# Kernel tuning notes

Hardware: AMD Instinct MI355X
Metric: run time of the kernel (lower is better)

Reference implementation:

```python
import jax, jax.numpy as jnp
import numpy as np

B, H, V, MSG_MAX_LEN = 16384, 512, 32, 20


def setup_inputs() -> dict:
    key = jax.random.key(0)
    ks = jax.random.split(key, 8)
    s = 0.05  # weight scale so softmax stays well-conditioned
    return {
        "encoder_hidden": jax.random.normal(ks[0], (B, H), jnp.float32),
        "encoder_cell": jax.random.normal(ks[1], (B, H), jnp.float32),
        "W_ih": jax.random.normal(ks[2], (4 * H, V), jnp.float32) * s,
        "b_ih": jax.random.normal(ks[3], (4 * H,), jnp.float32) * s,
        "W_hh": jax.random.normal(ks[4], (4 * H, H), jnp.float32) * s,
        "b_hh": jax.random.normal(ks[5], (4 * H,), jnp.float32) * s,
        "W_out": jax.random.normal(ks[6], (V, H), jnp.float32) * s,
        "b_out": jax.random.normal(ks[7], (V,), jnp.float32) * s,
        "init_input": jnp.zeros((1, V), jnp.float32),
        "eos_idx": 31,
    }


def reference(encoder_hidden, encoder_cell, W_ih, b_ih, W_hh, b_hh, W_out, b_out, init_input, eos_idx):
    batch = encoder_hidden.shape[0]
    vocab = W_out.shape[0]
    # Original code never updates decoder_input (typo 'deocder_input'), so the
    # LSTM input is init_input every step -> input projection is loop-invariant.
    x = jnp.broadcast_to(init_input, (batch, init_input.shape[1]))
    x_proj = x @ W_ih.T + b_ih  # [B, 4H]

    def step(carry, _):
        h, c, mask, lp = carry  # h,c: [B,H]; mask: [1,B]; lp: scalar
        mask_out = mask  # mask is appended BEFORE the update in the original
        gates = x_proj + h @ W_hh.T + b_hh
        i, f, g, o = jnp.split(gates, 4, axis=1)  # torch LSTMCell gate order i,f,g,o
        i = jax.nn.sigmoid(i); f = jax.nn.sigmoid(f)
        g = jnp.tanh(g); o = jax.nn.sigmoid(o)
        c = f * c + i * g
        h = o * jnp.tanh(c)
        probs = jax.nn.softmax(h @ W_out.T + b_out, axis=1)  # [B,V]
        predict = jax.nn.one_hot(jnp.argmax(probs, axis=1), vocab, dtype=probs.dtype)  # eval-mode branch
        lp = lp + jnp.log((probs * predict).sum(axis=1)) @ mask[0]
        new_mask = mask * (1.0 - predict[:, eos_idx])  # zero out finished sequences
        return (h, c, new_mask, lp), (predict, mask_out)

    init = (encoder_hidden, encoder_cell,
            jnp.ones((1, batch), encoder_hidden.dtype),
            jnp.zeros((), encoder_hidden.dtype))
    (_, _, _, log_probs), (message, mask) = jax.lax.scan(step, init, None, length=MSG_MAX_LEN)
    return message, mask, log_probs  # [L,B,V], [L,1,B], scalar
```

## Files before the change

kernel.cpp:

```cpp
#include <hip/hip_runtime.h>
#include <math.h>

#define BATCH 16384
#define HDIM  512
#define VOCAB 32
#define STEPS 20
#define G4    2048

typedef _Float16 f16;
typedef _Float16 f16x8 __attribute__((ext_vector_type(8)));
typedef float    f32x16 __attribute__((ext_vector_type(16)));

#define SH   256.0f
#define SW   1024.0f
#define SINV (1.0f / (SH * SW))


__device__ __forceinline__ void gload16(const void* g, void* l) {
#if defined(__has_builtin) && __has_builtin(__builtin_amdgcn_global_load_lds)
    __builtin_amdgcn_global_load_lds(
        (const __attribute__((address_space(1))) void*)g,
        (__attribute__((address_space(3))) void*)l, 16, 0, 0);
#else
    *(float4*)l = *(const float4*)g;
#endif
}

__device__ __forceinline__ float fsig(float x)  { return 1.0f / (1.0f + __expf(-x)); }
__device__ __forceinline__ float ftanh(float x) { return 1.0f - 2.0f / (__expf(2.0f * x) + 1.0f); }

__global__ void init_xb_kernel(const float* __restrict__ W_ih,
                               const float* __restrict__ b_ih,
                               const float* __restrict__ b_hh,
                               const float* __restrict__ x0,
                               float* __restrict__ xb) {
    int n = blockIdx.x * blockDim.x + threadIdx.x;
    if (n >= G4) return;
    float s = b_ih[n] + b_hh[n];
    const float* wr = W_ih + (size_t)n * VOCAB;
    #pragma unroll
    for (int v = 0; v < VOCAB; v++) s += wr[v] * x0[v];
    xb[n] = s;
}

__global__ void init_mask_kernel(float* __restrict__ mask) {
    int b = blockIdx.x * blockDim.x + threadIdx.x;
    if (b < BATCH) mask[b] = 1.0f;
}

__global__ void wimg_kernel(const float* __restrict__ W_hh,
                            f16* __restrict__ Wh, f16* __restrict__ Wl) {
    size_t g  = (size_t)blockIdx.x * 256 + threadIdx.x;
    int ln = g & 63;  size_t r = g >> 6;
    int gg = r & 3;   size_t r2 = r >> 2;
    int ks = r2 & 1;  size_t r3 = r2 >> 1;
    int kc = r3 & 15; int jb = (int)(r3 >> 4);
    int n = gg * 512 + jb * 32 + (ln & 31);
    int k = kc * 32 + ks * 16 + (ln >> 5) * 8;
    const float* s = W_hh + (size_t)n * HDIM + k;
    f16x8 vh, vl;
    #pragma unroll
    for (int i = 0; i < 8; i++) {
        float x = s[i] * SW;
        f16 h = (f16)x;
        vh[i] = h;
        vl[i] = (f16)(x - (float)h);
    }
    *(f16x8*)(Wh + g * 8) = vh;
    *(f16x8*)(Wl + g * 8) = vl;
}

__global__ void woutimg_kernel(const float* __restrict__ W_out,
                               f16* __restrict__ Oh, f16* __restrict__ Ol) {
    int g  = blockIdx.x * 256 + threadIdx.x;
    int ln = g & 63;
    int r  = g >> 6;
    int kc = r >> 1, ks = r & 1;
    int v  = ln & 31;
    int k  = kc * 32 + ks * 16 + (ln >> 5) * 8;
    const float* s = W_out + (size_t)v * HDIM + k;
    f16x8 vh, vl;
    #pragma unroll
    for (int i = 0; i < 8; i++) {
        float x = s[i] * SW;
        f16 h = (f16)x;
        vh[i] = h;
        vl[i] = (f16)(x - (float)h);
    }
    *(f16x8*)(Oh + (size_t)g * 8) = vh;
    *(f16x8*)(Ol + (size_t)g * 8) = vl;
}

__global__ void hT_init_kernel(const float* __restrict__ src,
                               f16* __restrict__ dh, f16* __restrict__ dl) {
    size_t g = (size_t)blockIdx.x * 256 + threadIdx.x;
    int ln = g & 63;  size_t r = g >> 6;
    int mb = (int)(r & 511); int kk = (int)(r >> 9);
    int m = mb * 32 + (ln & 31);
    int k = kk * 16 + (ln >> 5) * 8;
    const float* s = src + (size_t)m * HDIM + k;
    f16x8 vh, vl;
    #pragma unroll
    for (int i = 0; i < 8; i++) {
        float x = s[i] * SH;
        f16 h = (f16)x;
        vh[i] = h;
        vl[i] = (f16)(x - (float)h);
    }
    *(f16x8*)(dh + g * 8) = vh;
    *(f16x8*)(dl + g * 8) = vl;
}

__global__ __launch_bounds__(256, 2)
void gemm_cell_mfma(const f16* __restrict__ hT_h, const f16* __restrict__ hT_l,
                    f16* __restrict__ hTo_h, f16* __restrict__ hTo_l,
                    float* __restrict__ c,
                    const f16* __restrict__ Wimg_h, const f16* __restrict__ Wimg_l,
                    const float* __restrict__ xb) {
    __shared__ __align__(16) char smem_raw[34048];
    f16* Blds = (f16*)smem_raw;

    const int tid  = threadIdx.x;
    const int lane = tid & 63;
    const int wave = tid >> 6;
    const int wm   = wave;
    const int spw  = wave >> 1;
    const int ksw  = wave & 1;
    const int jb   = blockIdx.y;
    const int mb0  = blockIdx.x * 8;
    const int m0   = blockIdx.x * 256;
    const int j0   = jb * 32;
    const int half = lane >> 5;
    const int l31  = lane & 31;

    f32x16 acc[2][4];
    #pragma unroll
    for (int t = 0; t < 2; t++)
        #pragma unroll
        for (int g = 0; g < 4; g++)
            #pragma unroll
            for (int r = 0; r < 16; r++) acc[t][g][r] = 0.0f;

    const f16* bsrc0 = (spw ? Wimg_l : Wimg_h)
                     + ((size_t)jb * 128 + ksw * 4) * 512 + lane * 8;
    f16* bdst0 = Blds + (size_t)(spw * 8 + ksw * 4) * 512 + lane * 8;

    auto stage_b = [&](int kc, int buf) {
        const f16* s = bsrc0 + (size_t)kc * 4096;
        f16* d = bdst0 + buf * 16 * 512;
        #pragma unroll
        for (int g = 0; g < 4; g++)
            gload16(s + g * 512, d + g * 512);
    };

    const size_t abase0 = ((size_t)mb0 + wm * 2) * 512 + lane * 8;
    auto load_ah = [&](int kc, f16x8 (&dst)[2][2]) {
        #pragma unroll
        for (int ks = 0; ks < 2; ks++)
            #pragma unroll
            for (int t = 0; t < 2; t++)
                dst[ks][t] = *(const f16x8*)(hT_h + abase0
                               + (size_t)(kc * 2 + ks) * (512 * 512) + t * 512);
    };
    auto load_al = [&](int kc, f16x8 (&dst)[2][2]) {
        #pragma unroll
        for (int ks = 0; ks < 2; ks++)
            #pragma unroll
            for (int t = 0; t < 2; t++)
                dst[ks][t] = *(const f16x8*)(hT_l + abase0
                               + (size_t)(kc * 2 + ks) * (512 * 512) + t * 512);
    };

    auto compute = [&](f16x8 (&ah)[2][2], f16x8 (&al)[2][2], int buf) {
        #pragma unroll
        for (int ks = 0; ks < 2; ks++) {
            f16x8 bh[4], bl[4];
            #pragma unroll
            for (int g = 0; g < 4; g++) {
                bh[g] = *(const f16x8*)(Blds + (size_t)(buf * 16 + ks * 4 + g) * 512 + lane * 8);
                bl[g] = *(const f16x8*)(Blds + (size_t)(buf * 16 + 8 + ks * 4 + g) * 512 + lane * 8);
            }
            #pragma unroll
            for (int g = 0; g < 4; g++)
                #pragma unroll
                for (int t = 0; t < 2; t++) {
                    acc[t][g] = __builtin_amdgcn_mfma_f32_32x32x16_f16(ah[ks][t], bh[g], acc[t][g], 0, 0, 0);
                    acc[t][g] = __builtin_amdgcn_mfma_f32_32x32x16_f16(ah[ks][t], bl[g], acc[t][g], 0, 0, 0);
                }
            #pragma unroll
            for (int g = 0; g < 4; g++)
                #pragma unroll
                for (int t = 0; t < 2; t++)
                    acc[t][g] = __builtin_amdgcn_mfma_f32_32x32x16_f16(al[ks][t], bh[g], acc[t][g], 0, 0, 0);
        }
    };

    f16x8 ah0[2][2], ah1[2][2], al[2][2];
    stage_b(0, 0);
    load_ah(0, ah0);
    for (int kc2 = 0; kc2 < 8; kc2++) {
        const int kc = kc2 * 2;
        __syncthreads();
        stage_b(kc + 1, 1);
        load_ah(kc + 1, ah1);
        load_al(kc, al);
        compute(ah0, al, 0);
        __syncthreads();
        stage_b(kc + 2, 0);
        load_ah(kc + 2, ah0);
        load_al(kc + 1, al);
        compute(ah1, al, 1);
    }

    __syncthreads();
    unsigned int* hstage = (unsigned int*)smem_raw;

    const float xbi = xb[0 * HDIM + j0 + l31];
    const float xbf = xb[1 * HDIM + j0 + l31];
    const float xbg = xb[2 * HDIM + j0 + l31];
    const float xbo = xb[3 * HDIM + j0 + l31];
    #pragma unroll
    for (int t = 0; t < 2; t++) {
        #pragma unroll
        for (int reg = 0; reg < 16; reg++) {
            int row = (reg & 3) + 8 * (reg >> 2) + 4 * half;
            int ml  = wm * 64 + t * 32 + row;
            float gi = acc[t][0][reg] * SINV + xbi;
            float gf = acc[t][1][reg] * SINV + xbf;
            float gg = acc[t][2][reg] * SINV + xbg;
            float go = acc[t][3][reg] * SINV + xbo;
            float si = fsig(gi);
            float sf = fsig(gf);
            float tg = ftanh(gg);
            float so = fsig(go);
            size_t idx = (size_t)(m0 + ml) * HDIM + j0 + l31;
            float cn = sf * c[idx] + si * tg;
            c[idx] = cn;
            float hs = so * ftanh(cn) * SH;
            f16 hh = (f16)hs;
            f16 hl = (f16)(hs - (float)hh);
            union { f16 h[2]; unsigned int u; } pk;
            pk.h[0] = hh; pk.h[1] = hl;
            hstage[ml * 33 + l31] = pk.u;
        }
    }
    __syncthreads();

    #pragma unroll
    for (int s = 0; s < 4; s++) {
        int q   = tid + s * 256;
        int ksp = q >> 9;
        int mbl = (q >> 6) & 7;
        int ln  = q & 63;
        int mrow = mbl * 32 + (ln & 31);
        int jj8  = ksp * 16 + (ln >> 5) * 8;
        f16x8 vh, vl;
        #pragma unroll
        for (int i = 0; i < 8; i++) {
            union { unsigned int u; f16 h[2]; } pk;
            pk.u = hstage[mrow * 33 + jj8 + i];
            vh[i] = pk.h[0];
            vl[i] = pk.h[1];
        }
        size_t gq = ((size_t)(jb * 2 + ksp) * 512 + mb0 + mbl) * 64 + ln;
        *(f16x8*)(hTo_h + gq * 8) = vh;
        *(f16x8*)(hTo_l + gq * 8) = vl;
    }
}

__global__ __launch_bounds__(64)
void out_mfma(const f16* __restrict__ hTh, const f16* __restrict__ hTl,
              const f16* __restrict__ Oh, const f16* __restrict__ Ol,
              const float* __restrict__ b_out,
              float* __restrict__ mask,
              float* __restrict__ msg_t,
              float* __restrict__ maskout_t,
              float* __restrict__ lp_part,
              const int* __restrict__ eos_ptr) {
    const int lane = threadIdx.x;
    const int mb   = blockIdx.x;
    const int half = lane >> 5;
    const int l31  = lane & 31;

    f32x16 acc;
    #pragma unroll
    for (int r = 0; r < 16; r++) acc[r] = 0.0f;

    f16x8 ah[3][2], al[3][2], bh[3][2], bl[3][2];
    auto load_frags = [&](int kc, int buf) {
        #pragma unroll
        for (int ks = 0; ks < 2; ks++) {
            size_t ga = ((size_t)(kc * 2 + ks) * 512 + mb) * 64 + lane;
            size_t gb = ((size_t)(kc * 2 + ks)) * 64 + lane;
            ah[buf][ks] = *(const f16x8*)(hTh + ga * 8);
            al[buf][ks] = *(const f16x8*)(hTl + ga * 8);
            bh[buf][ks] = *(const f16x8*)(Oh + gb * 8);
            bl[buf][ks] = *(const f16x8*)(Ol + gb * 8);
        }
    };

    load_frags(0, 0);
    load_frags(1, 1);
    for (int kc = 0; kc < 16; kc++) {
        load_frags(kc + 2, (kc + 2) % 3);
        int b = kc % 3;
        #pragma unroll
        for (int ks = 0; ks < 2; ks++) {
            acc = __builtin_amdgcn_mfma_f32_32x32x16_f16(ah[b][ks], bh[b][ks], acc, 0, 0, 0);
            acc = __builtin_amdgcn_mfma_f32_32x32x16_f16(ah[b][ks], bl[b][ks], acc, 0, 0, 0);
            acc = __builtin_amdgcn_mfma_f32_32x32x16_f16(al[b][ks], bh[b][ks], acc, 0, 0, 0);
        }
    }

    const float bo  = b_out[l31];
    const int   eos = *eos_ptr;
    const int   m0  = mb * 32;
    float lpacc = 0.0f;

    #pragma unroll
    for (int reg = 0; reg < 16; reg++) {
        int row = (reg & 3) + 8 * (reg >> 2) + 4 * half;
        int m   = m0 + row;
        float logit = acc[reg] * SINV + bo;

        float mval = logit;
        int   midx = l31;
        #pragma unroll
        for (int off = 16; off > 0; off >>= 1) {
            float ov = __shfl_xor(mval, off, 32);
            int   oi = __shfl_xor(midx, off, 32);
            if (ov > mval || (ov == mval && oi < midx)) { mval = ov; midx = oi; }
        }
        float s = __expf(logit - mval);
        #pragma unroll
        for (int off = 16; off > 0; off >>= 1) s += __shfl_xor(s, off, 32);

        msg_t[(size_t)m * VOCAB + l31] = (l31 == midx) ? 1.0f : 0.0f;
        if (l31 == 0) {
            float mo = mask[m];
            maskout_t[m] = mo;
            lpacc += mo * (-__logf(s));
            if (midx == eos) mask[m] = 0.0f;
        }
    }
    lpacc += __shfl_xor(lpacc, 32);
    if (lane == 0) lp_part[mb] = lpacc;
}

__global__ void reduce_lp_kernel(const float* __restrict__ parts, int n,
                                 float* __restrict__ out) {
    __shared__ float sm[256];
    float s = 0.0f;
    for (int i = threadIdx.x; i < n; i += 256) s += parts[i];
    sm[threadIdx.x] = s;
    __syncthreads();
    for (int off = 128; off > 0; off >>= 1) {
        if (threadIdx.x < off) sm[threadIdx.x] += sm[threadIdx.x + off];
        __syncthreads();
    }
    if (threadIdx.x == 0) *out = sm[0];
}

extern "C" void kernel_launch(void* const* d_in, const int* in_sizes, int n_in,
                              void* d_out, int out_size, void* d_ws, size_t ws_size,
                              hipStream_t stream) {
    const float* enc_h  = (const float*)d_in[0];
    const float* enc_c  = (const float*)d_in[1];
    const float* W_ih   = (const float*)d_in[2];
    const float* b_ih   = (const float*)d_in[3];
    const float* W_hh   = (const float*)d_in[4];
    const float* b_hh   = (const float*)d_in[5];
    const float* W_out  = (const float*)d_in[6];
    const float* b_out  = (const float*)d_in[7];
    const float* x0     = (const float*)d_in[8];
    const int*   eosP   = (const int*)d_in[9];

    float* out     = (float*)d_out;
    float* msg     = out;
    float* maskout = out + (size_t)STEPS * BATCH * VOCAB;
    float* lp_out  = maskout + (size_t)STEPS * BATCH;

    const size_t NH = (size_t)BATCH * HDIM;
    char* w = (char*)d_ws;
    f16* hTh_a = (f16*)w;            w += NH * sizeof(f16);
    f16* hTl_a = (f16*)w;            w += NH * sizeof(f16);
    f16* hTh_b = (f16*)w;            w += NH * sizeof(f16);
    f16* hTl_b = (f16*)w;            w += NH * sizeof(f16);
    float* cbuf = (float*)w;         w += NH * sizeof(float);
    f16* Wimg_h = (f16*)w;           w += (size_t)G4 * HDIM * sizeof(f16);
    f16* Wimg_l = (f16*)w;           w += (size_t)G4 * HDIM * sizeof(f16);
    f16* Wout_h = (f16*)w;           w += (size_t)VOCAB * HDIM * sizeof(f16);
    f16* Wout_l = (f16*)w;           w += (size_t)VOCAB * HDIM * sizeof(f16);
    float* xb = (float*)w;           w += G4 * sizeof(float);
    float* maskbuf = (float*)w;      w += BATCH * sizeof(float);
    float* lp_parts = (float*)w;

    hipMemcpyAsync(cbuf, enc_c, NH * sizeof(float), hipMemcpyDeviceToDevice, stream);
    init_mask_kernel<<<(BATCH + 255) / 256, 256, 0, stream>>>(maskbuf);
    init_xb_kernel<<<(G4 + 255) / 256, 256, 0, stream>>>(W_ih, b_ih, b_hh, x0, xb);
    wimg_kernel<<<(G4 * HDIM / 8) / 256, 256, 0, stream>>>(W_hh, Wimg_h, Wimg_l);
    woutimg_kernel<<<8, 256, 0, stream>>>(W_out, Wout_h, Wout_l);
    hT_init_kernel<<<(int)((NH / 8) / 256), 256, 0, stream>>>(enc_h, hTh_a, hTl_a);

    for (int t = 0; t < STEPS; t++) {
        const f16* hi_in = (t & 1) ? hTh_b : hTh_a;
        const f16* lo_in = (t & 1) ? hTl_b : hTl_a;
        f16* hi_out      = (t & 1) ? hTh_a : hTh_b;
        f16* lo_out      = (t & 1) ? hTl_a : hTl_b;
        gemm_cell_mfma<<<dim3(BATCH / 256, HDIM / 32), 256, 0, stream>>>(
            hi_in, lo_in, hi_out, lo_out, cbuf, Wimg_h, Wimg_l, xb);
        out_mfma<<<BATCH / 32, 64, 0, stream>>>(
            hi_out, lo_out, Wout_h, Wout_l, b_out, maskbuf,
            msg + (size_t)t * BATCH * VOCAB,
            maskout + (size_t)t * BATCH,
            lp_parts + (size_t)t * (BATCH / 32),
            eosP);
    }
    reduce_lp_kernel<<<1, 256, 0, stream>>>(lp_parts, STEPS * (BATCH / 32), lp_out);
}
```

Before: 2.641 ms.

## Fuse output projection of previous step into next step's LSTM gemm launch

Merges the per-step gemm_cell and out_mfma kernels into one launch. Extra blocks compute the vocab projection, argmax and log-prob for step t-1 while the main blocks compute the LSTM cell for step t, since both only read the previous hidden state. This halves the launch count and lets the small, low-occupancy output work overlap the large GEMM. It also bounds the fragment prefetch in the output loop, which previously loaded past the last chunk, and reorders the MFMA issue order in the gemm. One trailing output launch handles the final step. The risk is that output blocks compete with gemm blocks for CUs.

Result: faster. 2.570 ms (-2.7%).

```diff
diff --git a/kernel.cpp b/kernel.cpp
--- a/kernel.cpp
+++ b/kernel.cpp
@@ -111,24 +111,116 @@
     *(f16x8*)(dl + g * 8) = vl;
 }
 
+__device__ __forceinline__ void out_body(int lane, int mb,
+        const f16* __restrict__ hTh, const f16* __restrict__ hTl,
+        const f16* __restrict__ Oh,  const f16* __restrict__ Ol,
+        const float* __restrict__ b_out,
+        float* __restrict__ mask, float* __restrict__ msg_t,
+        float* __restrict__ maskout_t, float* __restrict__ lp_part, int eos) {
+    const int half = lane >> 5;
+    const int l31  = lane & 31;
+
+    f32x16 acc;
+    #pragma unroll
+    for (int r = 0; r < 16; r++) acc[r] = 0.0f;
+
+    f16x8 ah[3][2], al[3][2], bh[3][2], bl[3][2];
+    auto load_frags = [&](int kc, int buf) {
+        #pragma unroll
+        for (int ks = 0; ks < 2; ks++) {
+            size_t ga = ((size_t)(kc * 2 + ks) * 512 + mb) * 64 + lane;
+            size_t gb = ((size_t)(kc * 2 + ks)) * 64 + lane;
+            ah[buf][ks] = *(const f16x8*)(hTh + ga * 8);
+            al[buf][ks] = *(const f16x8*)(hTl + ga * 8);
+            bh[buf][ks] = *(const f16x8*)(Oh + gb * 8);
+            bl[buf][ks] = *(const f16x8*)(Ol + gb * 8);
+        }
+    };
+
+    load_frags(0, 0);
+    load_frags(1, 1);
+    for (int kc = 0; kc < 16; kc++) {
+        if (kc < 14) load_frags(kc + 2, (kc + 2) % 3);
+        int b = kc % 3;
+        #pragma unroll
+        for (int ks = 0; ks < 2; ks++) {
+            acc = __builtin_amdgcn_mfma_f32_32x32x16_f16(ah[b][ks], bh[b][ks], acc, 0, 0, 0);
+            acc = __builtin_amdgcn_mfma_f32_32x32x16_f16(ah[b][ks], bl[b][ks], acc, 0, 0, 0);
+            acc = __builtin_amdgcn_mfma_f32_32x32x16_f16(al[b][ks], bh[b][ks], acc, 0, 0, 0);
+        }
+    }
+
+    const float bo = b_out[l31];
+    const int   m0 = mb * 32;
+    float lpacc = 0.0f;
+
+    #pragma unroll
+    for (int reg = 0; reg < 16; reg++) {
+        int row = (reg & 3) + 8 * (reg >> 2) + 4 * half;
+        int m   = m0 + row;
+        float logit = acc[reg] * SINV + bo;
+
+        float mval = logit;
+        int   midx = l31;
+        #pragma unroll
+        for (int off = 16; off > 0; off >>= 1) {
+            float ov = __shfl_xor(mval, off, 32);
+            int   oi = __shfl_xor(midx, off, 32);
+            if (ov > mval || (ov == mval && oi < midx)) { mval = ov; midx = oi; }
+        }
+        float s = __expf(logit - mval);
+        #pragma unroll
+        for (int off = 16; off > 0; off >>= 1) s += __shfl_xor(s, off, 32);
+
+        msg_t[(size_t)m * VOCAB + l31] = (l31 == midx) ? 1.0f : 0.0f;
+        if (l31 == 0) {
+            float mo = mask[m];
+            maskout_t[m] = mo;
+            lpacc += mo * (-__logf(s));
+            if (midx == eos) mask[m] = 0.0f;
+        }
+    }
+    lpacc += __shfl_xor(lpacc, 32);
+    if (lane == 0) lp_part[mb] = lpacc;
+}
+
 __global__ __launch_bounds__(256, 2)
-void gemm_cell_mfma(const f16* __restrict__ hT_h, const f16* __restrict__ hT_l,
-                    f16* __restrict__ hTo_h, f16* __restrict__ hTo_l,
-                    float* __restrict__ c,
-                    const f16* __restrict__ Wimg_h, const f16* __restrict__ Wimg_l,
-                    const float* __restrict__ xb) {
+void step_fused(const f16* __restrict__ hT_h, const f16* __restrict__ hT_l,
+                f16* __restrict__ hTo_h, f16* __restrict__ hTo_l,
+                float* __restrict__ c,
+                const f16* __restrict__ Wimg_h, const f16* __restrict__ Wimg_l,
+                const float* __restrict__ xb,
+                const f16* __restrict__ Oh, const f16* __restrict__ Ol,
+                const float* __restrict__ b_out,
+                float* __restrict__ mask,
+                float* __restrict__ msg_p,
+                float* __restrict__ maskout_p,
+                float* __restrict__ lp_p,
+                const int* __restrict__ eos_ptr,
+                int has_out) {
     __shared__ __align__(16) char smem_raw[34048];
     f16* Blds = (f16*)smem_raw;
 
     const int tid  = threadIdx.x;
     const int lane = tid & 63;
     const int wave = tid >> 6;
+    const int bid  = blockIdx.x;
+
+    if (bid >= 1024) {
+        if (!has_out) return;
+        int mb = (bid - 1024) * 4 + wave;
+        out_body(lane, mb, hT_h, hT_l, Oh, Ol, b_out,
+                 mask, msg_p, maskout_p, lp_p, *eos_ptr);
+        return;
+    }
+
     const int wm   = wave;
     const int spw  = wave >> 1;
     const int ksw  = wave & 1;
-    const int jb   = blockIdx.y;
-    const int mb0  = blockIdx.x * 8;
-    const int m0   = blockIdx.x * 256;
+    const int jb   = bid >> 6;
+    const int mt64 = bid & 63;
+    const int mb0  = mt64 * 8;
+    const int m0   = mt64 * 256;
     const int j0   = jb * 32;
     const int half = lane >> 5;
     const int l31  = lane & 31;
@@ -183,10 +275,13 @@
             #pragma unroll
             for (int g = 0; g < 4; g++)
                 #pragma unroll
-                for (int t = 0; t < 2; t++) {
+                for (int t = 0; t < 2; t++)
                     acc[t][g] = __builtin_amdgcn_mfma_f32_32x32x16_f16(ah[ks][t], bh[g], acc[t][g], 0, 0, 0);
+            #pragma unroll
+            for (int g = 0; g < 4; g++)
+                #pragma unroll
+                for (int t = 0; t < 2; t++)
                     acc[t][g] = __builtin_amdgcn_mfma_f32_32x32x16_f16(ah[ks][t], bl[g], acc[t][g], 0, 0, 0);
-                }
             #pragma unroll
             for (int g = 0; g < 4; g++)
                 #pragma unroll
@@ -277,74 +372,8 @@
               float* __restrict__ maskout_t,
               float* __restrict__ lp_part,
               const int* __restrict__ eos_ptr) {
-    const int lane = threadIdx.x;
-    const int mb   = blockIdx.x;
-    const int half = lane >> 5;
-    const int l31  = lane & 31;
-
-    f32x16 acc;
-    #pragma unroll
-    for (int r = 0; r < 16; r++) acc[r] = 0.0f;
-
-    f16x8 ah[3][2], al[3][2], bh[3][2], bl[3][2];
-    auto load_frags = [&](int kc, int buf) {
-        #pragma unroll
-        for (int ks = 0; ks < 2; ks++) {
-            size_t ga = ((size_t)(kc * 2 + ks) * 512 + mb) * 64 + lane;
-            size_t gb = ((size_t)(kc * 2 + ks)) * 64 + lane;
-            ah[buf][ks] = *(const f16x8*)(hTh + ga * 8);
-            al[buf][ks] = *(const f16x8*)(hTl + ga * 8);
-            bh[buf][ks] = *(const f16x8*)(Oh + gb * 8);
-            bl[buf][ks] = *(const f16x8*)(Ol + gb * 8);
-        }
-    };
-
-    load_frags(0, 0);
-    load_frags(1, 1);
-    for (int kc = 0; kc < 16; kc++) {
-        load_frags(kc + 2, (kc + 2) % 3);
-        int b = kc % 3;
-        #pragma unroll
-        for (int ks = 0; ks < 2; ks++) {
-            acc = __builtin_amdgcn_mfma_f32_32x32x16_f16(ah[b][ks], bh[b][ks], acc, 0, 0, 0);
-            acc = __builtin_amdgcn_mfma_f32_32x32x16_f16(ah[b][ks], bl[b][ks], acc, 0, 0, 0);
-            acc = __builtin_amdgcn_mfma_f32_32x32x16_f16(al[b][ks], bh[b][ks], acc, 0, 0, 0);
-        }
-    }
-
-    const float bo  = b_out[l31];
-    const int   eos = *eos_ptr;
-    const int   m0  = mb * 32;
-    float lpacc = 0.0f;
-
-    #pragma unroll
-    for (int reg = 0; reg < 16; reg++) {
-        int row = (reg & 3) + 8 * (reg >> 2) + 4 * half;
-        int m   = m0 + row;
-        float logit = acc[reg] * SINV + bo;
-
-        float mval = logit;
-        int   midx = l31;
-        #pragma unroll
-        for (int off = 16; off > 0; off >>= 1) {
-            float ov = __shfl_xor(mval, off, 32);
-            int   oi = __shfl_xor(midx, off, 32);
-            if (ov > mval || (ov == mval && oi < midx)) { mval = ov; midx = oi; }
-        }
-        float s = __expf(logit - mval);
-        #pragma unroll
-        for (int off = 16; off > 0; off >>= 1) s += __shfl_xor(s, off, 32);
-
-        msg_t[(size_t)m * VOCAB + l31] = (l31 == midx) ? 1.0f : 0.0f;
-        if (l31 == 0) {
-            float mo = mask[m];
-            maskout_t[m] = mo;
-            lpacc += mo * (-__logf(s));
-            if (midx == eos) mask[m] = 0.0f;
-        }
-    }
-    lpacc += __shfl_xor(lpacc, 32);
-    if (lane == 0) lp_part[mb] = lpacc;
+    out_body(threadIdx.x, blockIdx.x, hTh, hTl, Oh, Ol, b_out,
+             mask, msg_t, maskout_t, lp_part, *eos_ptr);
 }
 
 __global__ void reduce_lp_kernel(const float* __restrict__ parts, int n,
@@ -407,14 +436,24 @@
         const f16* lo_in = (t & 1) ? hTl_b : hTl_a;
         f16* hi_out      = (t & 1) ? hTh_a : hTh_b;
         f16* lo_out      = (t & 1) ? hTl_a : hTl_b;
-        gemm_cell_mfma<<<dim3(BATCH / 256, HDIM / 32), 256, 0, stream>>>(
-            hi_in, lo_in, hi_out, lo_out, cbuf, Wimg_h, Wimg_l, xb);
-        out_mfma<<<BATCH / 32, 64, 0, stream>>>(
-            hi_out, lo_out, Wout_h, Wout_l, b_out, maskbuf,
-            msg + (size_t)t * BATCH * VOCAB,
-            maskout + (size_t)t * BATCH,
-            lp_parts + (size_t)t * (BATCH / 32),
+        int tp = (t > 0) ? (t - 1) : 0;
+        step_fused<<<1152, 256, 0, stream>>>(
+            hi_in, lo_in, hi_out, lo_out, cbuf, Wimg_h, Wimg_l, xb,
+            Wout_h, Wout_l, b_out, maskbuf,
+            msg + (size_t)tp * BATCH * VOCAB,
+            maskout + (size_t)tp * BATCH,
+            lp_parts + (size_t)tp * 512,
+            eosP, t > 0 ? 1 : 0);
+    }
+    {
+        const f16* hi = (STEPS & 1) ? hTh_b : hTh_a;
+        const f16* lo = (STEPS & 1) ? hTl_b : hTl_a;
+        out_mfma<<<512, 64, 0, stream>>>(
+            hi, lo, Wout_h, Wout_l, b_out, maskbuf,
+            msg + (size_t)(STEPS - 1) * BATCH * VOCAB,
+            maskout + (size_t)(STEPS - 1) * BATCH,
+            lp_parts + (size_t)(STEPS - 1) * 512,
             eosP);
     }
-    reduce_lp_kernel<<<1, 256, 0, stream>>>(lp_parts, STEPS * (BATCH / 32), lp_out);
-}
+    reduce_lp_kernel<<<1, 256, 0, stream>>>(lp_parts, STEPS * 512, lp_out);
+}
```
